# Kernel optimization log

Measured on AMD Instinct MI355X. Metric: run time of the kernel, lower is better.

## Reference

```python
import jax, jax.numpy as jnp
import numpy as np

N_HEADS = 16


def setup_inputs() -> dict:
    key = jax.random.key(0)
    ks = jax.random.split(key, 7)
    B, S, E = 4, 2048, 1024
    s = 0.02
    return {
        "x": jax.random.normal(ks[0], (B, S, E), dtype=jnp.float32),
        "Wq": jax.random.normal(ks[1], (E, E), dtype=jnp.float32) * s,
        "bq": jax.random.normal(ks[2], (E,), dtype=jnp.float32) * s,
        "Wk": jax.random.normal(ks[3], (E, E), dtype=jnp.float32) * s,
        "bk": jax.random.normal(ks[4], (E,), dtype=jnp.float32) * s,
        "Wv": jax.random.normal(ks[5], (E, E), dtype=jnp.float32) * s,
        "bv": jax.random.normal(ks[6], (E,), dtype=jnp.float32) * s,
    }


def reference(x, Wq, bq, Wk, bk, Wv, bv):
    B, S, E = x.shape
    H = N_HEADS
    D = E // H  # att_dim
    scale = 1.0 / jnp.sqrt(jnp.asarray(D, dtype=x.dtype))
    # torch Linear: y = x @ W.T + b
    q = (x @ Wq.T + bq).reshape(B, S, H, D)
    k = (x @ Wk.T + bk).reshape(B, S, H, D)
    v = (x @ Wv.T + bv).reshape(B, S, H, D)
    # scores: [B, H, S, S]
    scores = jnp.einsum("bqhd,bkhd->bhqk", q, k) * scale
    attn = jax.nn.softmax(scores, axis=-1)
    out = jnp.einsum("bhqk,bkhd->bqhd", attn, v)
    return out.reshape(B, S, E)
```

## Files before the change

kernel.cpp:

```cpp
#include <hip/hip_runtime.h>
#include <stdint.h>
#include <math.h>

typedef __bf16 bf16;
typedef __attribute__((ext_vector_type(8))) __bf16 bf16x8;
typedef __attribute__((ext_vector_type(4))) float f32x4;
typedef unsigned short u16;
typedef unsigned int u32;

#define BATCH 4
#define SEQ   2048
#define EMB   1024
#define HEADS 16
#define HDIM  64
#define BH    (BATCH*HEADS)

#define QSCALE 0.125f

#define OFF_XB 0u
#define OFF_WC 16777216u
#define OFF_Q  23068672u
#define OFF_K  39845888u
#define OFF_VT 56623104u

#define DRAIN_VM asm volatile("s_waitcnt vmcnt(0)" ::: "memory")
#define FENCE_LDS do { \
    asm volatile("s_waitcnt lgkmcnt(0)" ::: "memory"); \
    __builtin_amdgcn_sched_barrier(0); \
} while (0)


__device__ __forceinline__ u16 f2bf(float f) {
    u32 b = __builtin_bit_cast(u32, f);
    return (u16)((b + 0x7fffu + ((b >> 16) & 1u)) >> 16);
}

__device__ __forceinline__ u32 cvt_pk_bf16(float a, float b) {
    u32 r;
    asm("v_cvt_pk_bf16_f32 %0, %1, %2" : "=v"(r) : "v"(a), "v"(b));
    return r;
}

__global__ void cvt_f32_bf16(const float* __restrict__ in, u16* __restrict__ out, int n4) {
    int i = blockIdx.x * blockDim.x + threadIdx.x;
    int stride = gridDim.x * blockDim.x;
    for (; i < n4; i += stride) {
        float4 v = reinterpret_cast<const float4*>(in)[i];
        ushort4 o;
        o.x = f2bf(v.x); o.y = f2bf(v.y); o.z = f2bf(v.z); o.w = f2bf(v.w);
        reinterpret_cast<ushort4*>(out)[i] = o;
    }
}

__global__ __launch_bounds__(256, 2) void qkv_gemm(
    const u16* __restrict__ xb, const u16* __restrict__ wc,
    const float* __restrict__ bq, const float* __restrict__ bk_, const float* __restrict__ bv,
    u16* __restrict__ Qw, u16* __restrict__ Kw, u16* __restrict__ Vt)
{
    __shared__ u16 lds[2 * 128 * 64];
    const int tid = threadIdx.x;
    const int w = tid >> 6, l = tid & 63;
    const int hi = l >> 4, lo = l & 15;
    const int bm = blockIdx.x & 63;
    const int bn = blockIdx.x >> 6;
    const int wm = w >> 1, wn = w & 1;

    const int srow   = l >> 3;
    const int schunk = (l & 7) ^ (srow & 7);

    f32x4 acc[4][4];
#pragma unroll
    for (int i = 0; i < 4; ++i)
#pragma unroll
        for (int j = 0; j < 4; ++j) acc[i][j] = f32x4{0.f, 0.f, 0.f, 0.f};

    for (int t = 0; t < 16; ++t) {
        const u16* asrc = xb + (size_t)(bm * 128 + srow) * 1024 + t * 64 + schunk * 8;
        const u16* bsrc = wc + (size_t)(bn * 128 + srow) * 1024 + t * 64 + schunk * 8;
#pragma unroll
        for (int i = 0; i < 4; ++i) {
            int c = i * 4 + w;
            __builtin_amdgcn_global_load_lds(
                (const __attribute__((address_space(1))) u32*)(asrc + (size_t)c * 8 * 1024),
                (__attribute__((address_space(3))) u32*)(&lds[c * 512]), 16, 0, 0);
            __builtin_amdgcn_global_load_lds(
                (const __attribute__((address_space(1))) u32*)(bsrc + (size_t)c * 8 * 1024),
                (__attribute__((address_space(3))) u32*)(&lds[128 * 64 + c * 512]), 16, 0, 0);
        }
        DRAIN_VM;
        __syncthreads();
#pragma unroll
        for (int kk = 0; kk < 2; ++kk) {
            bf16x8 af[4], bfr[4];
#pragma unroll
            for (int mt = 0; mt < 4; ++mt) {
                int row = wm * 64 + mt * 16 + lo;
                int off = (kk * 64 + hi * 16) ^ ((row & 7) << 4);
                af[mt] = *reinterpret_cast<const bf16x8*>((const char*)lds + row * 128 + off);
            }
#pragma unroll
            for (int nt = 0; nt < 4; ++nt) {
                int row = wn * 64 + nt * 16 + lo;
                int off = (kk * 64 + hi * 16) ^ ((row & 7) << 4);
                bfr[nt] = *reinterpret_cast<const bf16x8*>((const char*)lds + 128 * 64 * 2 + row * 128 + off);
            }
#pragma unroll
            for (int mt = 0; mt < 4; ++mt)
#pragma unroll
                for (int nt = 0; nt < 4; ++nt)
                    acc[mt][nt] = __builtin_amdgcn_mfma_f32_16x16x32_bf16(af[mt], bfr[nt], acc[mt][nt], 0, 0, 0);
        }
        __syncthreads();
    }

#pragma unroll
    for (int nt = 0; nt < 4; ++nt) {
        int ng  = bn * 128 + wn * 64 + nt * 16 + lo;
        int mat = ng >> 10;
        int nl  = ng & 1023;
        int h = nl >> 6, d = nl & 63;
        const float* bp = (mat == 0) ? bq : (mat == 1 ? bk_ : bv);
        float bias = bp[nl];
        float scl = (mat == 0) ? QSCALE : 1.0f;
#pragma unroll
        for (int mt = 0; mt < 4; ++mt) {
            int mbase = bm * 128 + wm * 64 + mt * 16 + hi * 4;
            int b = mbase >> 11, s = mbase & 2047;
            if (mat < 2) {
                u16* dst = (mat == 0) ? Qw : Kw;
                size_t base = ((size_t)(b * 16 + h) * 2048) * 64 + (size_t)d;
#pragma unroll
                for (int r = 0; r < 4; ++r)
                    dst[base + (size_t)(s + r) * 64] = f2bf((acc[mt][nt][r] + bias) * scl);
            } else {
                ushort4 o;
                o.x = f2bf(acc[mt][nt][0] + bias);
                o.y = f2bf(acc[mt][nt][1] + bias);
                o.z = f2bf(acc[mt][nt][2] + bias);
                o.w = f2bf(acc[mt][nt][3] + bias);
                *reinterpret_cast<ushort4*>(&Vt[((size_t)(b * 16 + h) * 64 + d) * 2048 + s]) = o;
            }
        }
    }
}

#define KVB 64
__global__ __launch_bounds__(256, 3) void attn(
    const u16* __restrict__ Qw, const u16* __restrict__ Kw, const u16* __restrict__ Vt,
    float* __restrict__ out)
{
    __shared__ char smem[51200];
    const int tid = threadIdx.x;
    const int w = tid >> 6, l = tid & 63;
    const int hi = (l >> 4) & 3, lo = l & 15;

    const int bid = blockIdx.x;
    const int xcd = bid & 7, ii = bid >> 3;
    const int bh = xcd * 8 + (ii & 7);
    const int qt = ii >> 3;
    const int bb = bh >> 4, h = bh & 15;
    const int q0w = qt * 128 + w * 32;

    const u16* Qb = Qw + ((size_t)bh * 2048 + q0w) * 64;
    const u16* Kb = Kw + (size_t)bh * 2048 * 64;
    const u16* Vb = Vt + (size_t)bh * 64 * 2048;
    char* bufs = smem;
    char* myP  = smem + 32768 + w * 4608;

    bf16x8 qf[2][2];
#pragma unroll
    for (int qs = 0; qs < 2; ++qs)
#pragma unroll
        for (int kc = 0; kc < 2; ++kc)
            qf[qs][kc] = *reinterpret_cast<const bf16x8*>(Qb + (qs * 16 + lo) * 64 + kc * 32 + hi * 8);

    const int r0 = w * 8 + (l >> 3);
    const int cs = (l & 7) ^ (r0 & 7);

    const f32x4 zf = {0.f, 0.f, 0.f, 0.f};
    f32x4 acc[4][2];
#pragma unroll
    for (int dt = 0; dt < 4; ++dt)
#pragma unroll
        for (int qs = 0; qs < 2; ++qs) acc[dt][qs] = zf;
    f32x4 psv[2] = {zf, zf};

#define STAGE(kvbase, dst)                                                              \
    {                                                                                   \
        _Pragma("unroll")                                                               \
        for (int s = 0; s < 2; ++s) {                                                   \
            const u16* srcK = Kb + (size_t)((kvbase) + s * 32 + r0) * 64 + cs * 8;      \
            __builtin_amdgcn_global_load_lds(                                           \
                (const __attribute__((address_space(1))) u32*)srcK,                     \
                (__attribute__((address_space(3))) u32*)((dst) + s * 4096 + w * 1024),  \
                16, 0, 0);                                                              \
            const u16* srcV = Vb + (size_t)(s * 32 + r0) * 2048 + (kvbase) + cs * 8;    \
            __builtin_amdgcn_global_load_lds(                                           \
                (const __attribute__((address_space(1))) u32*)srcV,                     \
                (__attribute__((address_space(3))) u32*)((dst) + 8192 + s * 4096 + w * 1024), \
                16, 0, 0);                                                              \
        }                                                                               \
    }

    STAGE(0, bufs);
    DRAIN_VM;
    __syncthreads();

    int buf = 0;
    for (int t = 0; t < 2048 / KVB; ++t) {
        if (t + 1 < 2048 / KVB) STAGE((t + 1) * KVB, bufs + (buf ^ 1) * 16384);

        const char* bK = bufs + buf * 16384;
        const char* bV = bK + 8192;

        f32x4 st[4][2];
#pragma unroll
        for (int ct = 0; ct < 4; ++ct) {
            int r = ct * 16 + lo;
            bf16x8 k0 = *reinterpret_cast<const bf16x8*>(bK + r * 128 + ((hi ^ (r & 7)) * 16));
            bf16x8 k1 = *reinterpret_cast<const bf16x8*>(bK + r * 128 + (((4 + hi) ^ (r & 7)) * 16));
#pragma unroll
            for (int qs = 0; qs < 2; ++qs) {
                f32x4 s4 = __builtin_amdgcn_mfma_f32_16x16x32_bf16(k0, qf[qs][0], zf, 0, 0, 0);
                st[ct][qs] = __builtin_amdgcn_mfma_f32_16x16x32_bf16(k1, qf[qs][1], s4, 0, 0, 0);
            }
        }
#pragma unroll
        for (int ct = 0; ct < 4; ++ct)
#pragma unroll
            for (int qs = 0; qs < 2; ++qs) {
                f32x4 p;
#pragma unroll
                for (int r = 0; r < 4; ++r) p[r] = __expf(st[ct][qs][r]);
                psv[qs] += p;
                uint2 pk;
                pk.x = cvt_pk_bf16(p[0], p[1]);
                pk.y = cvt_pk_bf16(p[2], p[3]);
                *reinterpret_cast<uint2*>(myP + (qs * 16 + lo) * 144 + ct * 32 + hi * 8) = pk;
            }
        FENCE_LDS;
#pragma unroll
        for (int hf = 0; hf < 2; ++hf) {
            bf16x8 pf[2];
#pragma unroll
            for (int qs = 0; qs < 2; ++qs)
                pf[qs] = *reinterpret_cast<const bf16x8*>(myP + (qs * 16 + lo) * 144 + hf * 64 + hi * 16);
#pragma unroll
            for (int dt = 0; dt < 4; ++dt) {
                int r = dt * 16 + lo;
                bf16x8 vf = *reinterpret_cast<const bf16x8*>(
                    bV + r * 128 + (((hf * 4 + hi) ^ (r & 7)) * 16));
#pragma unroll
                for (int qs = 0; qs < 2; ++qs)
                    acc[dt][qs] = __builtin_amdgcn_mfma_f32_16x16x32_bf16(vf, pf[qs], acc[dt][qs], 0, 0, 0);
            }
        }
        DRAIN_VM;
        __syncthreads();
        buf ^= 1;
    }
#undef STAGE

    float inv[2];
#pragma unroll
    for (int qs = 0; qs < 2; ++qs) {
        float s = psv[qs][0] + psv[qs][1] + psv[qs][2] + psv[qs][3];
        s += __shfl_xor(s, 16);
        s += __shfl_xor(s, 32);
        inv[qs] = 1.f / s;
    }

#pragma unroll
    for (int dt = 0; dt < 4; ++dt)
#pragma unroll
        for (int qs = 0; qs < 2; ++qs) {
            float* og = out + ((size_t)(bb * 2048 + q0w + qs * 16 + lo)) * 1024 + h * 64 + dt * 16 + hi * 4;
            float2 v01 = {acc[dt][qs][0] * inv[qs], acc[dt][qs][1] * inv[qs]};
            float2 v23 = {acc[dt][qs][2] * inv[qs], acc[dt][qs][3] * inv[qs]};
            *reinterpret_cast<float2*>(og)     = v01;
            *reinterpret_cast<float2*>(og + 2) = v23;
        }
}

extern "C" void kernel_launch(void* const* d_in, const int* in_sizes, int n_in,
                              void* d_out, int out_size, void* d_ws, size_t ws_size,
                              hipStream_t stream) {
    (void)in_sizes; (void)n_in; (void)out_size; (void)ws_size;
    const float* x  = (const float*)d_in[0];
    const float* Wq = (const float*)d_in[1];
    const float* bq = (const float*)d_in[2];
    const float* Wk = (const float*)d_in[3];
    const float* bk = (const float*)d_in[4];
    const float* Wv = (const float*)d_in[5];
    const float* bv = (const float*)d_in[6];
    float* out = (float*)d_out;
    char* ws = (char*)d_ws;

    u16* xb = (u16*)(ws + OFF_XB);
    u16* wc = (u16*)(ws + OFF_WC);
    u16* Qw = (u16*)(ws + OFF_Q);
    u16* Kw = (u16*)(ws + OFF_K);
    u16* Vt = (u16*)(ws + OFF_VT);

    cvt_f32_bf16<<<2048, 256, 0, stream>>>(x, xb, (BATCH * SEQ * EMB) / 4);
    cvt_f32_bf16<<<512, 256, 0, stream>>>(Wq, wc, (EMB * EMB) / 4);
    cvt_f32_bf16<<<512, 256, 0, stream>>>(Wk, wc + EMB * EMB, (EMB * EMB) / 4);
    cvt_f32_bf16<<<512, 256, 0, stream>>>(Wv, wc + 2 * EMB * EMB, (EMB * EMB) / 4);

    qkv_gemm<<<64 * 24, 256, 0, stream>>>(xb, wc, bq, bk, bv, Qw, Kw, Vt);
    attn<<<1024, 256, 0, stream>>>(Qw, Kw, Vt, out);
}
```

Baseline: 163.0 us.

## Widen attention blocks to eight waves and fuse conversion launches

After: 144.9 us. 1.13x faster.

```diff
diff --git a/kernel.cpp b/kernel.cpp
--- a/kernel.cpp
+++ b/kernel.cpp
@@ -41,14 +41,24 @@
     return r;
 }
 
-__global__ void cvt_f32_bf16(const float* __restrict__ in, u16* __restrict__ out, int n4) {
-    int i = blockIdx.x * blockDim.x + threadIdx.x;
+__global__ void cvt_all(const float* __restrict__ x,
+                        const float* __restrict__ wq, const float* __restrict__ wk,
+                        const float* __restrict__ wv,
+                        u16* __restrict__ xb, u16* __restrict__ wc) {
+    const int X4 = (BATCH * SEQ * EMB) / 4;
+    const int W4 = (EMB * EMB) / 4;
+    const int n4 = X4 + 3 * W4;
     int stride = gridDim.x * blockDim.x;
-    for (; i < n4; i += stride) {
-        float4 v = reinterpret_cast<const float4*>(in)[i];
+    for (int i = blockIdx.x * blockDim.x + threadIdx.x; i < n4; i += stride) {
+        const float* src; u16* dst; int j;
+        if (i < X4)              { src = x;  dst = xb;                j = i; }
+        else if (i < X4 + W4)    { src = wq; dst = wc;                j = i - X4; }
+        else if (i < X4 + 2*W4)  { src = wk; dst = wc + EMB * EMB;    j = i - X4 - W4; }
+        else                     { src = wv; dst = wc + 2 * EMB * EMB; j = i - X4 - 2 * W4; }
+        float4 v = reinterpret_cast<const float4*>(src)[j];
         ushort4 o;
         o.x = f2bf(v.x); o.y = f2bf(v.y); o.z = f2bf(v.z); o.w = f2bf(v.w);
-        reinterpret_cast<ushort4*>(out)[i] = o;
+        reinterpret_cast<ushort4*>(dst)[j] = o;
     }
 }
 
@@ -145,21 +155,21 @@
 }
 
 #define KVB 64
-__global__ __launch_bounds__(256, 3) void attn(
+__global__ __launch_bounds__(512, 4) void attn(
     const u16* __restrict__ Qw, const u16* __restrict__ Kw, const u16* __restrict__ Vt,
     float* __restrict__ out)
 {
-    __shared__ char smem[51200];
+    __shared__ char smem[69632];
     const int tid = threadIdx.x;
     const int w = tid >> 6, l = tid & 63;
-    const int hi = (l >> 4) & 3, lo = l & 15;
+    const int hi = l >> 4, lo = l & 15;
 
     const int bid = blockIdx.x;
     const int xcd = bid & 7, ii = bid >> 3;
     const int bh = xcd * 8 + (ii & 7);
     const int qt = ii >> 3;
     const int bb = bh >> 4, h = bh & 15;
-    const int q0w = qt * 128 + w * 32;
+    const int q0w = qt * 256 + w * 32;
 
     const u16* Qb = Qw + ((size_t)bh * 2048 + q0w) * 64;
     const u16* Kb = Kw + (size_t)bh * 2048 * 64;
@@ -185,21 +195,17 @@
         for (int qs = 0; qs < 2; ++qs) acc[dt][qs] = zf;
     f32x4 psv[2] = {zf, zf};
 
-#define STAGE(kvbase, dst)                                                              \
-    {                                                                                   \
-        _Pragma("unroll")                                                               \
-        for (int s = 0; s < 2; ++s) {                                                   \
-            const u16* srcK = Kb + (size_t)((kvbase) + s * 32 + r0) * 64 + cs * 8;      \
-            __builtin_amdgcn_global_load_lds(                                           \
-                (const __attribute__((address_space(1))) u32*)srcK,                     \
-                (__attribute__((address_space(3))) u32*)((dst) + s * 4096 + w * 1024),  \
-                16, 0, 0);                                                              \
-            const u16* srcV = Vb + (size_t)(s * 32 + r0) * 2048 + (kvbase) + cs * 8;    \
-            __builtin_amdgcn_global_load_lds(                                           \
-                (const __attribute__((address_space(1))) u32*)srcV,                     \
-                (__attribute__((address_space(3))) u32*)((dst) + 8192 + s * 4096 + w * 1024), \
-                16, 0, 0);                                                              \
-        }                                                                               \
+#define STAGE(kvbase, dst)                                                          \
+    {                                                                               \
+        const u16* srcK = Kb + (size_t)((kvbase) + r0) * 64 + cs * 8;               \
+        __builtin_amdgcn_global_load_lds(                                           \
+            (const __attribute__((address_space(1))) u32*)srcK,                     \
+            (__attribute__((address_space(3))) u32*)((dst) + w * 1024), 16, 0, 0);  \
+        const u16* srcV = Vb + (size_t)r0 * 2048 + (kvbase) + cs * 8;               \
+        __builtin_amdgcn_global_load_lds(                                           \
+            (const __attribute__((address_space(1))) u32*)srcV,                     \
+            (__attribute__((address_space(3))) u32*)((dst) + 8192 + w * 1024),      \
+            16, 0, 0);                                                              \
     }
 
     STAGE(0, bufs);
@@ -302,11 +308,7 @@
     u16* Kw = (u16*)(ws + OFF_K);
     u16* Vt = (u16*)(ws + OFF_VT);
 
-    cvt_f32_bf16<<<2048, 256, 0, stream>>>(x, xb, (BATCH * SEQ * EMB) / 4);
-    cvt_f32_bf16<<<512, 256, 0, stream>>>(Wq, wc, (EMB * EMB) / 4);
-    cvt_f32_bf16<<<512, 256, 0, stream>>>(Wk, wc + EMB * EMB, (EMB * EMB) / 4);
-    cvt_f32_bf16<<<512, 256, 0, stream>>>(Wv, wc + 2 * EMB * EMB, (EMB * EMB) / 4);
-
+    cvt_all<<<2048, 256, 0, stream>>>(x, Wq, Wk, Wv, xb, wc);
     qkv_gemm<<<64 * 24, 256, 0, stream>>>(xb, wc, bq, bk, bv, Qw, Kw, Vt);
-    attn<<<1024, 256, 0, stream>>>(Qw, Kw, Vt, out);
-}
+    attn<<<512, 512, 0, stream>>>(Qw, Kw, Vt, out);
+}
```
